# Kernel optimization log

Hardware: AMD Instinct MI355X
Metric: run time of the kernel (lower is better)

## Reference

```python
import jax, jax.numpy as jnp
import numpy as np

N_NODES = 100000
N_EDGES = 1600000
IN_CH = 256
OUT_CH = 64
ITERATIONS = 4


def setup_inputs() -> dict:
    key = jax.random.key(0)
    k1, k2, k3, k4, k5 = jax.random.split(key, 5)
    adj_index = jax.random.randint(k1, (2, N_EDGES), 0, N_NODES, dtype=jnp.int64)
    adj_values = jax.random.uniform(k2, (N_EDGES,), dtype=jnp.float32)
    features = jax.random.normal(k3, (N_NODES, IN_CH), dtype=jnp.float32)
    # Xavier-uniform init as in the torch module
    bw = float(np.sqrt(6.0 / (IN_CH + OUT_CH)))
    weight = jax.random.uniform(k4, (IN_CH, OUT_CH), dtype=jnp.float32, minval=-bw, maxval=bw)
    bb = float(np.sqrt(6.0 / (1 + OUT_CH)))
    bias = jax.random.uniform(k5, (1, OUT_CH), dtype=jnp.float32, minval=-bb, maxval=bb)
    return {"adj_index": adj_index, "adj_values": adj_values, "features": features,
            "weight": weight, "bias": bias}


def reference(adj_index, adj_values, features, weight, bias):
    # Dense transform: [N, in] @ [in, out] + [1, out], then ReLU (dropout = identity in eval)
    base = jax.nn.relu(features @ weight + bias)  # [N, out]
    rows = adj_index[0]  # destination rows of A (output index of SpMM)
    cols = adj_index[1]  # source columns of A (gather index)
    n = base.shape[0]
    # (iterations - 1) hops of SpMM: base <- A @ base
    for _ in range(ITERATIONS - 1):
        msgs = adj_values[:, None] * base[cols]           # [E, out] gather + scale
        base = jax.ops.segment_sum(msgs, rows, num_segments=n)  # [N, out] scatter-add
    return base
```

## Files before the change

### kernel.cpp

```cpp
#include <hip/hip_runtime.h>

#define IN_CH 256
#define OUT_CH 64
#define NFMAX 512
#define RPB 256
#define CHUNK 6144
#define CAP 8192

__device__ __forceinline__ unsigned short f2bf(float f) {
    unsigned u = __float_as_uint(f);
    u += 0x7fff + ((u >> 16) & 1);
    return (unsigned short)(u >> 16);
}
__device__ __forceinline__ float bf2f(unsigned short h) {
    return __uint_as_float((unsigned)h << 16);
}

struct Edge12 { int r; int c; float v; };

using bfrag = __attribute__((ext_vector_type(8))) short;
using ffrag = __attribute__((ext_vector_type(4))) float;

__global__ __launch_bounds__(256) void gemm_mfma_kernel(
    const float* __restrict__ feat, const float* __restrict__ W,
    const float* __restrict__ bias, unsigned short* __restrict__ out, int n)
{
    __shared__ unsigned short Wl[IN_CH * OUT_CH / 8 * 8];

    for (int i = threadIdx.x; i < IN_CH * OUT_CH; i += 256) {
        int k  = i >> 6;
        int c  = i & 63;
        int ks = k >> 5;
        int kq = (k >> 3) & 3;
        int j  = k & 7;
        int nt = c >> 4;
        int lc = c & 15;
        Wl[(((ks * 4 + nt) * 64) + kq * 16 + lc) * 8 + j] = f2bf(W[i]);
    }
    __syncthreads();

    const int wv   = threadIdx.x >> 6;
    const int lane = threadIdx.x & 63;
    const int quad = lane >> 4;
    const int lc   = lane & 15;

    const int arow = blockIdx.x * 64 + wv * 16 + lc;
    const int lrow = min(arow, n - 1);
    const float4* frow = (const float4*)(feat + (size_t)lrow * IN_CH);

    ffrag acc[4];
#pragma unroll
    for (int nt = 0; nt < 4; ++nt)
#pragma unroll
        for (int r = 0; r < 4; ++r) acc[nt][r] = 0.f;

#pragma unroll
    for (int ks = 0; ks < 8; ++ks) {
        const int k0 = ks * 32;
        float4 a0 = frow[(k0 >> 2) + quad * 2 + 0];
        float4 a1 = frow[(k0 >> 2) + quad * 2 + 1];
        bfrag af;
        af[0] = (short)f2bf(a0.x); af[1] = (short)f2bf(a0.y);
        af[2] = (short)f2bf(a0.z); af[3] = (short)f2bf(a0.w);
        af[4] = (short)f2bf(a1.x); af[5] = (short)f2bf(a1.y);
        af[6] = (short)f2bf(a1.z); af[7] = (short)f2bf(a1.w);
#pragma unroll
        for (int nt = 0; nt < 4; ++nt) {
            bfrag bf = *(const bfrag*)&Wl[(((ks * 4 + nt) * 64) + lane) * 8];
            acc[nt] = __builtin_amdgcn_mfma_f32_16x16x32_bf16(af, bf, acc[nt], 0, 0, 0);
        }
    }

#pragma unroll
    for (int nt = 0; nt < 4; ++nt) {
        float bv = bias[nt * 16 + lc];
#pragma unroll
        for (int r = 0; r < 4; ++r) {
            int orow = blockIdx.x * 64 + wv * 16 + quad * 4 + r;
            if (orow < n) {
                float v = fmaxf(acc[nt][r] + bv, 0.f);
                out[(size_t)orow * OUT_CH + nt * 16 + lc] = f2bf(v);
            }
        }
    }
}


__global__ __launch_bounds__(256) void fine_count_kernel(
    const int* __restrict__ rows, int* __restrict__ fineCnt,
    int nEdges, int nfine)
{
    __shared__ int h[NFMAX];
    const int t = threadIdx.x;
    for (int i = t; i < nfine; i += 256) h[i] = 0;
    __syncthreads();
    const int stride = gridDim.x * 256;
    for (int e = blockIdx.x * 256 + t; e < nEdges; e += stride)
        atomicAdd(&h[__builtin_nontemporal_load(rows + e) >> 8], 1);
    __syncthreads();
    for (int i = t; i < nfine; i += 256) {
        int v = h[i];
        if (v) atomicAdd(&fineCnt[i], v);
    }
}

__global__ __launch_bounds__(256) void fine_scan_kernel(
    const int* __restrict__ fineCnt, int* __restrict__ fineBase,
    int* __restrict__ flushCursor, int* __restrict__ rowptr,
    int n, int nfine, int E)
{
    __shared__ int tmp[256];
    const int t = threadIdx.x;
    int a = (2 * t     < nfine) ? fineCnt[2 * t]     : 0;
    int b = (2 * t + 1 < nfine) ? fineCnt[2 * t + 1] : 0;
    tmp[t] = a + b;
    __syncthreads();
    for (int off = 1; off < 256; off <<= 1) {
        int x = (t >= off) ? tmp[t - off] : 0;
        __syncthreads();
        tmp[t] += x;
        __syncthreads();
    }
    int excl = tmp[t] - (a + b);
    if (2 * t < nfine)     { fineBase[2 * t]     = excl;     flushCursor[2 * t]     = excl;     }
    if (2 * t + 1 < nfine) { fineBase[2 * t + 1] = excl + a; flushCursor[2 * t + 1] = excl + a; }
    if (t == 0) { fineBase[nfine] = E; rowptr[n] = E; }
}

__global__ __launch_bounds__(256) void fine_scatter_kernel(
    const int* __restrict__ rows, const int* __restrict__ cols,
    const float* __restrict__ vals, int* __restrict__ flushCursor,
    Edge12* __restrict__ eb, int nEdges, int nfine)
{
    __shared__ int hist[NFMAX];
    __shared__ int lofs[NFMAX];
    __shared__ int gpos[NFMAX];
    __shared__ int cur[NFMAX];
    __shared__ int scanTmp[256];
    __shared__ int   sr[CHUNK];
    __shared__ int   sc[CHUNK];
    __shared__ float sv[CHUNK];

    const int t  = threadIdx.x;
    const int e0 = blockIdx.x * CHUNK;
    const int cnt_in = min(CHUNK, nEdges - e0);

    for (int i = t; i < nfine; i += 256) hist[i] = 0;
    __syncthreads();

    int   lr[CHUNK / 256];
    int   lc[CHUNK / 256];
    float lv[CHUNK / 256];
#pragma unroll
    for (int j = 0; j < CHUNK / 256; ++j) {
        int i = j * 256 + t;
        if (i < cnt_in) {
            lr[j] = __builtin_nontemporal_load(rows + e0 + i);
            lc[j] = __builtin_nontemporal_load(cols + e0 + i);
            lv[j] = __builtin_nontemporal_load(vals + e0 + i);
            atomicAdd(&hist[lr[j] >> 8], 1);
        } else {
            lr[j] = -1;
        }
    }
    __syncthreads();

    int a  = (2 * t     < nfine) ? hist[2 * t]     : 0;
    int b2 = (2 * t + 1 < nfine) ? hist[2 * t + 1] : 0;
    scanTmp[t] = a + b2;
    __syncthreads();
    for (int off = 1; off < 256; off <<= 1) {
        int x = (t >= off) ? scanTmp[t - off] : 0;
        __syncthreads();
        scanTmp[t] += x;
        __syncthreads();
    }
    int excl = scanTmp[t] - (a + b2);
    if (2 * t < nfine)     lofs[2 * t]     = excl;
    if (2 * t + 1 < nfine) lofs[2 * t + 1] = excl + a;
    __syncthreads();

    for (int i = t; i < nfine; i += 256) {
        int h = hist[i];
        gpos[i] = h ? atomicAdd(&flushCursor[i], h) : 0;
        cur[i]  = lofs[i];
    }
    __syncthreads();

#pragma unroll
    for (int j = 0; j < CHUNK / 256; ++j) {
        if (lr[j] >= 0) {
            int bk = lr[j] >> 8;
            int p  = atomicAdd(&cur[bk], 1);
            sr[p] = lr[j];
            sc[p] = lc[j];
            sv[p] = lv[j];
        }
    }
    __syncthreads();

    for (int i = t; i < cnt_in; i += 256) {
        int bk = sr[i] >> 8;
        int p  = gpos[bk] + (i - lofs[bk]);
        eb[p].r = sr[i];
        eb[p].c = sc[i];
        eb[p].v = sv[i];
    }
}

__global__ __launch_bounds__(256) void bucket_sort_kernel(
    const Edge12* __restrict__ eb, const int* __restrict__ fineBase,
    int2* __restrict__ spack, int* __restrict__ rowptr, int n)
{
    __shared__ int  rowCnt[RPB];
    __shared__ int  rowStart[RPB + 1];
    __shared__ int  scanTmp[RPB];
    __shared__ int  winEnd;
    __shared__ int2 st[CAP];

    const int bkt = blockIdx.x;
    const int t   = threadIdx.x;
    const int lo  = fineBase[bkt];
    const int hi  = fineBase[bkt + 1];
    const int r0  = bkt << 8;

    rowCnt[t] = 0;
    __syncthreads();
    for (int e = lo + t; e < hi; e += 256)
        atomicAdd(&rowCnt[eb[e].r - r0], 1);
    __syncthreads();

    int v = rowCnt[t];
    scanTmp[t] = v;
    __syncthreads();
    for (int off = 1; off < 256; off <<= 1) {
        int x = (t >= off) ? scanTmp[t - off] : 0;
        __syncthreads();
        scanTmp[t] += x;
        __syncthreads();
    }
    rowStart[t + 1] = scanTmp[t];
    if (t == 0) rowStart[0] = 0;
    __syncthreads();

    if (r0 + t < n) rowptr[r0 + t] = lo + rowStart[t];

    int rs = 0;
    while (rs < RPB) {
        if (t == 0) {
            int base = rowStart[rs];
            if (rowStart[rs + 1] - base > CAP) {
                winEnd = -(rs + 1);
            } else {
                int re = rs;
                while (re < RPB && rowStart[re + 1] - base <= CAP) ++re;
                winEnd = re;
            }
        }
        __syncthreads();
        int  re     = winEnd;
        bool direct = false;
        if (re < 0) { re = -re; direct = true; }
        const int base = rowStart[rs];
        const int cnt  = rowStart[re] - base;

        if (t >= rs && t < re) rowCnt[t] = rowStart[t] - base;
        __syncthreads();

        if (!direct) {
            for (int e = lo + t; e < hi; e += 256) {
                Edge12 ed = eb[e];
                int rl = ed.r - r0;
                if (rl >= rs && rl < re) {
                    int p = atomicAdd(&rowCnt[rl], 1);
                    st[p] = make_int2(ed.c, __float_as_int(ed.v));
                }
            }
            __syncthreads();
            for (int i = t; i < cnt; i += 256)
                spack[lo + base + i] = st[i];
        } else {
            for (int e = lo + t; e < hi; e += 256) {
                Edge12 ed = eb[e];
                if (ed.r - r0 == rs) {
                    int p = atomicAdd(&rowCnt[rs], 1);
                    spack[lo + base + p] = make_int2(ed.c, __float_as_int(ed.v));
                }
            }
        }
        __syncthreads();
        rs = re;
    }
}

template<bool DST_F32>
__global__ __launch_bounds__(256) void spmm_csr_kernel(
    const int* __restrict__ rowptr, const int2* __restrict__ spack,
    const unsigned short* __restrict__ src, void* __restrict__ dstv, int n)
{
    const int row  = blockIdx.x * 4 + (threadIdx.x >> 6);
    const int lane = threadIdx.x & 63;
    if (row >= n) return;

    const int beg = rowptr[row];
    const int end = rowptr[row + 1];
    const int sub = lane >> 4;
    const int ch  = (lane & 15) * 4;

    float4 acc0 = make_float4(0.f, 0.f, 0.f, 0.f);
    float4 acc1 = make_float4(0.f, 0.f, 0.f, 0.f);

    for (int b = beg; b < end; b += 16) {
        int e0 = b + sub;
        int e1 = b + 4 + sub;
        int e2 = b + 8 + sub;
        int e3 = b + 12 + sub;
        int2 p0 = spack[min(e0, end - 1)];
        int2 p1 = spack[min(e1, end - 1)];
        int2 p2 = spack[min(e2, end - 1)];
        int2 p3 = spack[min(e3, end - 1)];
        float v0 = (e0 < end) ? __int_as_float(p0.y) : 0.f;
        float v1 = (e1 < end) ? __int_as_float(p1.y) : 0.f;
        float v2 = (e2 < end) ? __int_as_float(p2.y) : 0.f;
        float v3 = (e3 < end) ? __int_as_float(p3.y) : 0.f;
        ushort4 s0 = *(const ushort4*)(src + ((size_t)p0.x << 6) + ch);
        ushort4 s1 = *(const ushort4*)(src + ((size_t)p1.x << 6) + ch);
        ushort4 s2 = *(const ushort4*)(src + ((size_t)p2.x << 6) + ch);
        ushort4 s3 = *(const ushort4*)(src + ((size_t)p3.x << 6) + ch);
        acc0.x = fmaf(v0, bf2f(s0.x), acc0.x);
        acc0.y = fmaf(v0, bf2f(s0.y), acc0.y);
        acc0.z = fmaf(v0, bf2f(s0.z), acc0.z);
        acc0.w = fmaf(v0, bf2f(s0.w), acc0.w);
        acc1.x = fmaf(v1, bf2f(s1.x), acc1.x);
        acc1.y = fmaf(v1, bf2f(s1.y), acc1.y);
        acc1.z = fmaf(v1, bf2f(s1.z), acc1.z);
        acc1.w = fmaf(v1, bf2f(s1.w), acc1.w);
        acc0.x = fmaf(v2, bf2f(s2.x), acc0.x);
        acc0.y = fmaf(v2, bf2f(s2.y), acc0.y);
        acc0.z = fmaf(v2, bf2f(s2.z), acc0.z);
        acc0.w = fmaf(v2, bf2f(s2.w), acc0.w);
        acc1.x = fmaf(v3, bf2f(s3.x), acc1.x);
        acc1.y = fmaf(v3, bf2f(s3.y), acc1.y);
        acc1.z = fmaf(v3, bf2f(s3.z), acc1.z);
        acc1.w = fmaf(v3, bf2f(s3.w), acc1.w);
    }

    float4 acc = make_float4(acc0.x + acc1.x, acc0.y + acc1.y,
                             acc0.z + acc1.z, acc0.w + acc1.w);

#pragma unroll
    for (int mask = 16; mask <= 32; mask <<= 1) {
        acc.x += __shfl_xor(acc.x, mask);
        acc.y += __shfl_xor(acc.y, mask);
        acc.z += __shfl_xor(acc.z, mask);
        acc.w += __shfl_xor(acc.w, mask);
    }

    if (lane < 16) {
        if constexpr (DST_F32) {
            *(float4*)((float*)dstv + ((size_t)row << 6) + ch) = acc;
        } else {
            ushort4 o;
            o.x = f2bf(acc.x);
            o.y = f2bf(acc.y);
            o.z = f2bf(acc.z);
            o.w = f2bf(acc.w);
            *(ushort4*)((unsigned short*)dstv + ((size_t)row << 6) + ch) = o;
        }
    }
}

extern "C" void kernel_launch(void* const* d_in, const int* in_sizes, int n_in,
                              void* d_out, int out_size, void* d_ws, size_t ws_size,
                              hipStream_t stream)
{
    const int*   adj  = (const int*)d_in[0];
    const float* vals = (const float*)d_in[1];
    const float* feat = (const float*)d_in[2];
    const float* W    = (const float*)d_in[3];
    const float* bias = (const float*)d_in[4];

    const int E = in_sizes[1];
    const int n = in_sizes[2] / IN_CH;
    const int* rows = adj;
    const int* cols = adj + E;

    const int nfine = (n + RPB - 1) >> 8;

    char* ws = (char*)d_ws;
    size_t off = 0;
    auto alloc = [&](size_t bytes) {
        void* p = ws + off;
        off += (bytes + 255) & ~(size_t)255;
        return p;
    };
    unsigned short* B0 = (unsigned short*)alloc((size_t)n * OUT_CH * sizeof(unsigned short));
    unsigned short* B1 = (unsigned short*)alloc((size_t)n * OUT_CH * sizeof(unsigned short));
    int*   rowptr      = (int*)  alloc((size_t)(n + 1) * sizeof(int));
    int2*  spack       = (int2*) alloc((size_t)E * sizeof(int2));
    int*   fineCnt     = (int*)  alloc(NFMAX * sizeof(int));
    int*   fineBase    = (int*)  alloc((NFMAX + 1) * sizeof(int));
    int*   flushCursor = (int*)  alloc(NFMAX * sizeof(int));

    Edge12* eb = (Edge12*)B0;

    float* out = (float*)d_out;

    hipMemsetAsync(fineCnt, 0, (size_t)nfine * sizeof(int), stream);
    fine_count_kernel<<<256, 256, 0, stream>>>(rows, fineCnt, E, nfine);
    fine_scan_kernel<<<1, 256, 0, stream>>>(fineCnt, fineBase, flushCursor,
                                            rowptr, n, nfine, E);
    fine_scatter_kernel<<<(E + CHUNK - 1) / CHUNK, 256, 0, stream>>>(
        rows, cols, vals, flushCursor, eb, E, nfine);
    bucket_sort_kernel<<<nfine, 256, 0, stream>>>(eb, fineBase, spack, rowptr, n);

    gemm_mfma_kernel<<<(n + 63) / 64, 256, 0, stream>>>(feat, W, bias, B0, n);

    const int hblocks = (n + 3) / 4;
    spmm_csr_kernel<false><<<hblocks, 256, 0, stream>>>(rowptr, spack, B0, B1, n);
    spmm_csr_kernel<false><<<hblocks, 256, 0, stream>>>(rowptr, spack, B1, B0, n);
    spmm_csr_kernel<true><<<hblocks, 256, 0, stream>>>(rowptr, spack, B0, out, n);
}
```

Measured before the change: 396.1 us.

## Pre-swizzle weights once, double rows per wave, use hardware bf16 convert

Adds a small kernel that converts the weight matrix to bf16 in MFMA fragment order once, instead of every GEMM block doing that conversion and staging it through LDS. The GEMM now has each wave compute 32 rows with two accumulator sets that share each B fragment, which halves the block count and reads B directly from global memory (likely cached). It also swaps the manual float-to-bf16 rounding for the library conversion in the GEMM and SpMM paths. The costs are an extra kernel launch, higher register pressure, and B fragments coming through global or cache loads rather than LDS.

```diff
diff --git a/kernel.cpp b/kernel.cpp
--- a/kernel.cpp
+++ b/kernel.cpp
@@ -1,4 +1,5 @@
 #include <hip/hip_runtime.h>
+#include <hip/hip_bf16.h>
 
 #define IN_CH 256
 #define OUT_CH 64
@@ -12,6 +13,12 @@
     u += 0x7fff + ((u >> 16) & 1);
     return (unsigned short)(u >> 16);
 }
+__device__ __forceinline__ unsigned short f2bf_hw(float f) {
+    __hip_bfloat16 h = __float2bfloat16(f);
+    union { __hip_bfloat16 b; unsigned short u; } c;
+    c.b = h;
+    return c.u;
+}
 __device__ __forceinline__ float bf2f(unsigned short h) {
     return __uint_as_float((unsigned)h << 16);
 }
@@ -21,53 +28,61 @@
 using bfrag = __attribute__((ext_vector_type(8))) short;
 using ffrag = __attribute__((ext_vector_type(4))) float;
 
+__global__ __launch_bounds__(256) void wprep_kernel(
+    const float* __restrict__ W, unsigned short* __restrict__ Wf)
+{
+    int i = blockIdx.x * 256 + threadIdx.x;
+    int k  = i >> 6;
+    int c  = i & 63;
+    int ks = k >> 5;
+    int kq = (k >> 3) & 3;
+    int j  = k & 7;
+    int nt = c >> 4;
+    int lc = c & 15;
+    Wf[(((ks * 4 + nt) * 64) + kq * 16 + lc) * 8 + j] = f2bf(W[i]);
+}
+
 __global__ __launch_bounds__(256) void gemm_mfma_kernel(
-    const float* __restrict__ feat, const float* __restrict__ W,
+    const float* __restrict__ feat, const unsigned short* __restrict__ Wf,
     const float* __restrict__ bias, unsigned short* __restrict__ out, int n)
 {
-    __shared__ unsigned short Wl[IN_CH * OUT_CH / 8 * 8];
-
-    for (int i = threadIdx.x; i < IN_CH * OUT_CH; i += 256) {
-        int k  = i >> 6;
-        int c  = i & 63;
-        int ks = k >> 5;
-        int kq = (k >> 3) & 3;
-        int j  = k & 7;
-        int nt = c >> 4;
-        int lc = c & 15;
-        Wl[(((ks * 4 + nt) * 64) + kq * 16 + lc) * 8 + j] = f2bf(W[i]);
-    }
-    __syncthreads();
-
     const int wv   = threadIdx.x >> 6;
     const int lane = threadIdx.x & 63;
     const int quad = lane >> 4;
     const int lc   = lane & 15;
 
-    const int arow = blockIdx.x * 64 + wv * 16 + lc;
-    const int lrow = min(arow, n - 1);
-    const float4* frow = (const float4*)(feat + (size_t)lrow * IN_CH);
-
-    ffrag acc[4];
+    const int rbase = blockIdx.x * 128 + wv * 32;
+    const int lrow0 = min(rbase + lc,      n - 1);
+    const int lrow1 = min(rbase + 16 + lc, n - 1);
+    const float4* frow0 = (const float4*)(feat + (size_t)lrow0 * IN_CH);
+    const float4* frow1 = (const float4*)(feat + (size_t)lrow1 * IN_CH);
+
+    ffrag acc0[4], acc1[4];
 #pragma unroll
     for (int nt = 0; nt < 4; ++nt)
 #pragma unroll
-        for (int r = 0; r < 4; ++r) acc[nt][r] = 0.f;
+        for (int r = 0; r < 4; ++r) { acc0[nt][r] = 0.f; acc1[nt][r] = 0.f; }
 
 #pragma unroll
     for (int ks = 0; ks < 8; ++ks) {
-        const int k0 = ks * 32;
-        float4 a0 = frow[(k0 >> 2) + quad * 2 + 0];
-        float4 a1 = frow[(k0 >> 2) + quad * 2 + 1];
-        bfrag af;
-        af[0] = (short)f2bf(a0.x); af[1] = (short)f2bf(a0.y);
-        af[2] = (short)f2bf(a0.z); af[3] = (short)f2bf(a0.w);
-        af[4] = (short)f2bf(a1.x); af[5] = (short)f2bf(a1.y);
-        af[6] = (short)f2bf(a1.z); af[7] = (short)f2bf(a1.w);
+        float4 a00 = frow0[ks * 8 + quad * 2 + 0];
+        float4 a01 = frow0[ks * 8 + quad * 2 + 1];
+        float4 a10 = frow1[ks * 8 + quad * 2 + 0];
+        float4 a11 = frow1[ks * 8 + quad * 2 + 1];
+        bfrag af0, af1;
+        af0[0] = (short)f2bf_hw(a00.x); af0[1] = (short)f2bf_hw(a00.y);
+        af0[2] = (short)f2bf_hw(a00.z); af0[3] = (short)f2bf_hw(a00.w);
+        af0[4] = (short)f2bf_hw(a01.x); af0[5] = (short)f2bf_hw(a01.y);
+        af0[6] = (short)f2bf_hw(a01.z); af0[7] = (short)f2bf_hw(a01.w);
+        af1[0] = (short)f2bf_hw(a10.x); af1[1] = (short)f2bf_hw(a10.y);
+        af1[2] = (short)f2bf_hw(a10.z); af1[3] = (short)f2bf_hw(a10.w);
+        af1[4] = (short)f2bf_hw(a11.x); af1[5] = (short)f2bf_hw(a11.y);
+        af1[6] = (short)f2bf_hw(a11.z); af1[7] = (short)f2bf_hw(a11.w);
 #pragma unroll
         for (int nt = 0; nt < 4; ++nt) {
-            bfrag bf = *(const bfrag*)&Wl[(((ks * 4 + nt) * 64) + lane) * 8];
-            acc[nt] = __builtin_amdgcn_mfma_f32_16x16x32_bf16(af, bf, acc[nt], 0, 0, 0);
+            bfrag bf = *(const bfrag*)&Wf[(((ks * 4 + nt) * 64) + lane) * 8];
+            acc0[nt] = __builtin_amdgcn_mfma_f32_16x16x32_bf16(af0, bf, acc0[nt], 0, 0, 0);
+            acc1[nt] = __builtin_amdgcn_mfma_f32_16x16x32_bf16(af1, bf, acc1[nt], 0, 0, 0);
         }
     }
 
@@ -76,15 +91,19 @@
         float bv = bias[nt * 16 + lc];
 #pragma unroll
         for (int r = 0; r < 4; ++r) {
-            int orow = blockIdx.x * 64 + wv * 16 + quad * 4 + r;
-            if (orow < n) {
-                float v = fmaxf(acc[nt][r] + bv, 0.f);
-                out[(size_t)orow * OUT_CH + nt * 16 + lc] = f2bf(v);
+            int orow0 = rbase + quad * 4 + r;
+            int orow1 = rbase + 16 + quad * 4 + r;
+            if (orow0 < n) {
+                float v = fmaxf(acc0[nt][r] + bv, 0.f);
+                out[(size_t)orow0 * OUT_CH + nt * 16 + lc] = f2bf_hw(v);
             }
-        }
-    }
-}
-
+            if (orow1 < n) {
+                float v = fmaxf(acc1[nt][r] + bv, 0.f);
+                out[(size_t)orow1 * OUT_CH + nt * 16 + lc] = f2bf_hw(v);
+            }
+        }
+    }
+}
 
 __global__ __launch_bounds__(256) void fine_count_kernel(
     const int* __restrict__ rows, int* __restrict__ fineCnt,
@@ -361,10 +380,10 @@
             *(float4*)((float*)dstv + ((size_t)row << 6) + ch) = acc;
         } else {
             ushort4 o;
-            o.x = f2bf(acc.x);
-            o.y = f2bf(acc.y);
-            o.z = f2bf(acc.z);
-            o.w = f2bf(acc.w);
+            o.x = f2bf_hw(acc.x);
+            o.y = f2bf_hw(acc.y);
+            o.z = f2bf_hw(acc.z);
+            o.w = f2bf_hw(acc.w);
             *(ushort4*)((unsigned short*)dstv + ((size_t)row << 6) + ch) = o;
         }
     }
@@ -401,10 +420,13 @@
     int*   fineCnt     = (int*)  alloc(NFMAX * sizeof(int));
     int*   fineBase    = (int*)  alloc((NFMAX + 1) * sizeof(int));
     int*   flushCursor = (int*)  alloc(NFMAX * sizeof(int));
+    unsigned short* Wf = (unsigned short*)alloc((size_t)IN_CH * OUT_CH * sizeof(unsigned short));
 
     Edge12* eb = (Edge12*)B0;
 
     float* out = (float*)d_out;
+
+    wprep_kernel<<<(IN_CH * OUT_CH) / 256, 256, 0, stream>>>(W, Wf);
 
     hipMemsetAsync(fineCnt, 0, (size_t)nfine * sizeof(int), stream);
     fine_count_kernel<<<256, 256, 0, stream>>>(rows, fineCnt, E, nfine);
@@ -414,7 +436,7 @@
         rows, cols, vals, flushCursor, eb, E, nfine);
     bucket_sort_kernel<<<nfine, 256, 0, stream>>>(eb, fineBase, spack, rowptr, n);
 
-    gemm_mfma_kernel<<<(n + 63) / 64, 256, 0, stream>>>(feat, W, bias, B0, n);
+    gemm_mfma_kernel<<<(n + 127) / 128, 256, 0, stream>>>(feat, Wf, bias, B0, n);
 
     const int hblocks = (n + 3) / 4;
     spmm_csr_kernel<false><<<hblocks, 256, 0, stream>>>(rowptr, spack, B0, B1, n);
```

Result: no change. 390.7 us (-1.4%).
